# Kernel tuning notes

Hardware: AMD Instinct MI355X
Metric: run time of the kernel (lower is better)

The kernel has to match this reference:

```python
import jax, jax.numpy as jnp
import numpy as np

# ---- model constants (match init_kwargs) ----
N_USERS = 100_000
N_ITEMS = 50_000
N_ENTITIES = 200_000          # items are entities [0, N_ITEMS)
N_REL = 20                    # relations after the +1 shift; rel_weight has N_REL-1 rows
EMB = 64
HOPS = 2
MARGIN_CCL = 0.8
NUM_NEG = 64
ANGLE_W = 0.1
ANGLE_DROP = 0.5              # eval-mode Dropout(ones)*rate == constant rate scaling
N_EDGES = 1_000_000
NNZ = 1_000_000
N_TRIPLETS = 200_000
BATCH = 4096
EPS = 1e-6


def _l2norm(x):
    # torch F.normalize(dim=-1, eps=1e-12)
    return x / jnp.maximum(jnp.linalg.norm(x, axis=-1, keepdims=True), 1e-12)


def setup_inputs() -> dict:
    key = jax.random.key(0)
    ks = jax.random.split(key, 13)
    # xavier_uniform bounds: sqrt(6/(fan_in+fan_out))
    b_all = float(np.sqrt(6.0 / (N_USERS + N_ENTITIES + EMB)))
    b_cf = float(np.sqrt(6.0 / (N_ITEMS + EMB)))
    b_rel = float(np.sqrt(6.0 / (N_REL - 1 + EMB)))
    all_embed = jax.random.uniform(ks[0], (N_USERS + N_ENTITIES, EMB), jnp.float32, -b_all, b_all)
    item_emb_cf = jax.random.uniform(ks[1], (N_ITEMS, EMB), jnp.float32, -b_cf, b_cf)
    rel_weight = jax.random.uniform(ks[2], (N_REL - 1, EMB), jnp.float32, -b_rel, b_rel)
    # D^{-1/2} A row-normalized positive values
    interact_vals = jax.random.uniform(ks[3], (NNZ,), jnp.float32, 0.01, 0.3)
    user = jax.random.randint(ks[4], (BATCH,), 0, N_USERS)
    pos_item = jax.random.randint(ks[5], (BATCH,), 0, N_ITEMS)
    neg_item = jax.random.randint(ks[6], (BATCH, NUM_NEG), 0, N_ITEMS)
    edge_index = jax.random.randint(ks[7], (2, N_EDGES), 0, N_ENTITIES)
    edge_type = jax.random.randint(ks[8], (N_EDGES,), 1, N_REL)  # relations already +1 shifted
    interact_rows = jax.random.randint(ks[9], (NNZ,), 0, N_USERS)
    interact_cols = jax.random.randint(ks[10], (NNZ,), 0, N_ITEMS)  # URM cols live in item range
    triplet_h = jax.random.randint(ks[11], (N_TRIPLETS,), 0, N_ENTITIES)
    triplet_t = jax.random.randint(ks[12], (N_TRIPLETS,), 0, N_ITEMS)
    return dict(all_embed=all_embed, item_emb_cf=item_emb_cf, rel_weight=rel_weight,
                interact_vals=interact_vals, user=user, pos_item=pos_item, neg_item=neg_item,
                edge_index=edge_index, edge_type=edge_type, interact_rows=interact_rows,
                interact_cols=interact_cols, triplet_h=triplet_h, triplet_t=triplet_t)


def _gcn(user_emb, entity_emb, item_cf, rel_weight, edge_index, edge_type, rows, cols, vals):
    """Multi-hop HAKG GraphConv: relation-gated KG scatter-mean + sparse user/CF aggregation."""
    head, tail = edge_index[0], edge_index[1]
    ent_res, usr_res, cf_res = entity_emb, user_emb, item_cf
    cnt = jax.ops.segment_sum(jnp.ones(head.shape, entity_emb.dtype), head, N_ENTITIES)
    denom = jnp.maximum(cnt, 1.0)[:, None]            # scatter_mean denominator
    rel_e = rel_weight[edge_type - 1]                 # [E, D]
    for _ in range(HOPS):
        # KG aggregate: entity_agg[h] = mean_{(h,r,t)} entity[t] * rel[r]
        neigh = entity_emb[tail] * rel_e              # [E, D]
        entity_agg = jax.ops.segment_sum(neigh, head, N_ENTITIES) / denom
        # user aggregate: sparse interact_mat @ entity_emb
        user_agg = jax.ops.segment_sum(vals[:, None] * entity_emb[cols], rows, N_USERS)
        # CF branch (LightGCN-style): R @ item_cf then R^T @ (...)
        u_cf = jax.ops.segment_sum(vals[:, None] * item_cf[cols], rows, N_USERS)
        item_agg_cf = jax.ops.segment_sum(vals[:, None] * u_cf[rows], cols, N_ITEMS)
        entity_emb = _l2norm(entity_agg)
        user_emb = _l2norm(user_agg)
        item_cf = _l2norm(item_agg_cf)
        ent_res = ent_res + entity_emb
        usr_res = usr_res + user_emb
        cf_res = cf_res + item_cf
    return ent_res, usr_res, cf_res


def _half_aperture(u):
    K = 0.1
    sqnu = jnp.clip(jnp.sum(u * u, -1), 0.0, 1.0 - EPS)
    return jnp.arcsin(jnp.clip(K * (1.0 - sqnu) / jnp.sqrt(sqnu), -1.0 + EPS, 1.0 - EPS))


def _angle_at_u(u, v):
    nu = jnp.linalg.norm(u, axis=-1)
    nv = jnp.linalg.norm(v, axis=-1)
    dp = jnp.sum(u * v, -1)
    ed = jnp.linalg.norm(u - v, axis=-1)
    num = dp * (1.0 + nu ** 2) - nu ** 2 * (1.0 + nv ** 2)
    den = nu * ed * jnp.sqrt(jnp.clip(1.0 + nv ** 2 * nu ** 2 - 2.0 * dp, EPS, None)) + EPS
    return jnp.arccos(jnp.clip(num / den, -1.0 + EPS, 1.0 - EPS))


def _contrastive_loss(u_e, pos_e, neg_e, pos_cf, neg_cf):
    B = u_e.shape[0]
    u, p, n = _l2norm(u_e), _l2norm(pos_e), _l2norm(neg_e)
    pcf, ncf = _l2norm(pos_cf), _l2norm(neg_cf)
    ui_pos = jax.nn.relu(2.0 - (jnp.sum(u * p, -1) + jnp.sum(u * pcf, -1)))
    ub = jnp.repeat(u, NUM_NEG, axis=0)               # [B*K, D]
    def neg_loss(nn_):
        s = jax.nn.relu(jnp.sum(ub * nn_, -1) - MARGIN_CCL).reshape(B, NUM_NEG)
        return jnp.sum(s, -1) / (jnp.sum(s > 0, -1).astype(s.dtype) + 1e-5)
    return jnp.mean(ui_pos + neg_loss(n) + neg_loss(ncf))


def reference(all_embed, item_emb_cf, rel_weight, interact_vals, user, pos_item, neg_item,
              edge_index, edge_type, interact_rows, interact_cols, triplet_h, triplet_t):
    user_emb = all_embed[:N_USERS]
    entity_emb = all_embed[N_USERS:]
    ent_g, usr_g, cf_g = _gcn(user_emb, entity_emb, item_emb_cf, rel_weight,
                              edge_index, edge_type, interact_rows, interact_cols, interact_vals)
    flat_neg = neg_item.reshape(-1)
    u_e = usr_g[user]
    loss1 = _contrastive_loss(u_e, ent_g[pos_item], ent_g[flat_neg], cf_g[pos_item], cf_g[flat_neg])
    # angle (hierarchy) loss, vectorized over all cross-type triplets
    hs = entity_emb[triplet_h] * ANGLE_DROP
    ts = entity_emb[triplet_t] * ANGLE_DROP
    angle_half = jax.nn.relu(_angle_at_u(hs, ts) - _half_aperture(hs))
    loss2 = ANGLE_W * jnp.sum(angle_half) / N_TRIPLETS
    return loss1 + loss2
```

## Files before the change

### kernel.cpp

```cpp
#include <hip/hip_runtime.h>
#include <math.h>

#define N_USERS    100000
#define N_ITEMS    50000
#define N_ENTITIES 200000
#define N_REL      20
#define EMB        64
#define HOPS       2
#define MARGIN_CCL 0.8f
#define NUM_NEG    64
#define ANGLE_W    0.1f
#define ANGLE_DROP 0.5f
#define N_EDGES    1000000
#define NNZ        1000000
#define N_TRIPLETS 200000
#define BATCH      4096
#define EPSF       1e-6f

#define TILE1 4096
#define NBUCK 196
#define BCAP  9216
#define ACAP  8192
#define HBLK  ((N_EDGES + TILE1 - 1) / TILE1)
#define KGB   (N_ENTITIES / 32)
#define USERB (N_USERS / 16)
#define ITEMB ((N_ITEMS + 31) / 32)
#define ANGB  (N_TRIPLETS / 32)
#define LOSSB (BATCH / 4)
#define CONVE (N_ENTITIES * 16 / 256)
#define CONVI (N_ITEMS * 16 / 256)

typedef _Float16 half4_t __attribute__((ext_vector_type(4)));
typedef _Float16 half8_t __attribute__((ext_vector_type(8)));
typedef float float8_t __attribute__((ext_vector_type(8)));

__device__ inline float4 h2f(half4_t h) {
    return make_float4((float)h.x, (float)h.y, (float)h.z, (float)h.w);
}
__device__ inline half4_t f2h(float4 f) {
    half4_t h; h.x = (_Float16)f.x; h.y = (_Float16)f.y;
    h.z = (_Float16)f.z; h.w = (_Float16)f.w; return h;
}
__device__ inline float8_t h8_to_f8(half8_t h) { return __builtin_convertvector(h, float8_t); }
__device__ inline half8_t f8_to_h8(float8_t f) { return __builtin_convertvector(f, half8_t); }
__device__ inline half8_t h8_zero() {
    half8_t z;
    #pragma unroll
    for (int i = 0; i < 8; ++i) z[i] = (_Float16)0.0f;
    return z;
}
__device__ inline float sum_sq8(float8_t f) {
    float s = 0.f;
    #pragma unroll
    for (int i = 0; i < 8; ++i) s += f[i] * f[i];
    return s;
}
__device__ inline float dot8(float8_t a, float8_t b) {
    float s = 0.f;
    #pragma unroll
    for (int i = 0; i < 8; ++i) s += a[i] * b[i];
    return s;
}
__device__ inline float8_t f8_from2(float4 lo, float4 hi) {
    float8_t f;
    f[0] = lo.x; f[1] = lo.y; f[2] = lo.z; f[3] = lo.w;
    f[4] = hi.x; f[5] = hi.y; f[6] = hi.z; f[7] = hi.w;
    return f;
}
__device__ inline float grp_red8(float v) {
    v += __shfl_xor(v, 1, 64); v += __shfl_xor(v, 2, 64); v += __shfl_xor(v, 4, 64);
    return v;
}
__device__ inline float dot4(float4 a, float4 b) {
    return a.x * b.x + a.y * b.y + a.z * b.z + a.w * b.w;
}
__device__ inline float grp_red16(float v) {
    v += __shfl_xor(v, 1, 64); v += __shfl_xor(v, 2, 64);
    v += __shfl_xor(v, 4, 64); v += __shfl_xor(v, 8, 64);
    return v;
}
__device__ inline float cross_grp_scalar(float v) {
    v += __shfl_xor(v, 16, 64); v += __shfl_xor(v, 32, 64);
    return v;
}

__global__ void __launch_bounds__(256) prep_kernel(
        const float4* __restrict__ ent0, const float4* __restrict__ cf0,
        half4_t* __restrict__ ent_a, half4_t* __restrict__ comb_a,
        int* __restrict__ bcur_e, int* __restrict__ bcur_u, int* __restrict__ bcur_i) {
    int bx = blockIdx.x, t = threadIdx.x;
    if (bx < CONVE) { int i = bx * 256 + t; ent_a[i] = f2h(ent0[i]); return; }
    bx -= CONVE;
    if (bx < CONVI) {
        int i = bx * 256 + t;
        int row = i >> 4, o4 = i & 15;
        comb_a[row * 32 + o4] = f2h(ent0[i]);
        return;
    }
    bx -= CONVI;
    if (bx < CONVI) {
        int i = bx * 256 + t;
        int row = i >> 4, o4 = i & 15;
        comb_a[row * 32 + 16 + o4] = f2h(cf0[i]);
        return;
    }
    if (t < NBUCK) {
        bcur_e[t] = t * ACAP;
        bcur_u[t] = t * ACAP;
        bcur_i[t] = t * ACAP;
    }
}

__global__ void __launch_bounds__(256) phase1_all(
        const int* __restrict__ head, const int* __restrict__ tail,
        const int* __restrict__ etype, const int* __restrict__ rows,
        const int* __restrict__ cols, const float* __restrict__ vals,
        int* __restrict__ bcur_e, int* __restrict__ bcur_u, int* __restrict__ bcur_i,
        int* __restrict__ keys_e, int* __restrict__ kg_pay,
        int* __restrict__ keys_u, int2* __restrict__ u_pay,
        int* __restrict__ keys_i, int2* __restrict__ i_pay) {
    __shared__ int lhist[256], lstart[256], lcur[256], gbase[256];
    __shared__ int key_st[TILE1];
    __shared__ int2 pay_st[TILE1];
    int seg = blockIdx.x / HBLK;
    int tb  = blockIdx.x % HBLK;
    int t = threadIdx.x;
    int tstart = tb * TILE1;
    int valid = min(TILE1, N_EDGES - tstart);
    const int* karr = (seg == 0) ? head : (seg == 1) ? rows : cols;
    int shift = (seg == 0) ? 10 : (seg == 1) ? 9 : 8;
    int* bcur = (seg == 0) ? bcur_e : (seg == 1) ? bcur_u : bcur_i;
    lhist[t] = 0;
    __syncthreads();
    for (int i = t; i < valid; i += 256) atomicAdd(&lhist[karr[tstart + i] >> shift], 1);
    __syncthreads();
    int v = lhist[t];
    lstart[t] = v;
    __syncthreads();
    for (int d = 1; d < 256; d <<= 1) {
        int x = (t >= d) ? lstart[t - d] : 0;
        __syncthreads();
        lstart[t] += x;
        __syncthreads();
    }
    int excl = lstart[t] - v;
    lstart[t] = excl;
    lcur[t] = excl;
    gbase[t] = atomicAdd(&bcur[t], v);
    __syncthreads();
    if (seg == 0) {
        int* ps = (int*)pay_st;
        for (int i = t; i < valid; i += 256) {
            int h = head[tstart + i];
            int p = tail[tstart + i] | ((etype[tstart + i] - 1) << 18);
            int sp = atomicAdd(&lcur[h >> 10], 1);
            key_st[sp] = h;
            ps[sp] = p;
        }
        __syncthreads();
        for (int j = t; j < valid; j += 256) {
            int k = key_st[j];
            int b = k >> 10;
            int pos = gbase[b] + (j - lstart[b]);
            keys_e[pos] = k;
            kg_pay[pos] = ps[j];
        }
    } else {
        const int* oth = (seg == 1) ? cols : rows;
        int* keys = (seg == 1) ? keys_u : keys_i;
        int2* pay = (seg == 1) ? u_pay : i_pay;
        for (int i = t; i < valid; i += 256) {
            int k = karr[tstart + i];
            int2 p = make_int2(oth[tstart + i], __float_as_int(vals[tstart + i]));
            int sp = atomicAdd(&lcur[k >> shift], 1);
            key_st[sp] = k;
            pay_st[sp] = p;
        }
        __syncthreads();
        for (int j = t; j < valid; j += 256) {
            int k = key_st[j];
            int b = k >> shift;
            int pos = gbase[b] + (j - lstart[b]);
            keys[pos] = k;
            pay[pos] = pay_st[j];
        }
    }
}

__global__ void __launch_bounds__(256) phase2_all(
        const int* __restrict__ bcur_e, const int* __restrict__ keys_e,
        int* __restrict__ kg_pay, int* __restrict__ off_e,
        const int* __restrict__ bcur_u, const int* __restrict__ keys_u,
        int2* __restrict__ u_pay, int* __restrict__ off_u,
        const int* __restrict__ bcur_i, const int* __restrict__ keys_i,
        int2* __restrict__ i_pay, int* __restrict__ off_i) {
    __shared__ int hist[1024];
    __shared__ int s[256];
    __shared__ int2 lout2[BCAP];
    int seg = blockIdx.x / NBUCK;
    int b   = blockIdx.x % NBUCK;
    int t = threadIdx.x;
    int bins  = (seg == 0) ? 1024 : (seg == 1) ? 512 : 256;
    int shift = (seg == 0) ? 10 : (seg == 1) ? 9 : 8;
    int n_rows = (seg == 0) ? N_ENTITIES : (seg == 1) ? N_USERS : N_ITEMS;
    const int* bcur = (seg == 0) ? bcur_e : (seg == 1) ? bcur_u : bcur_i;
    const int* keys = (seg == 0) ? keys_e : (seg == 1) ? keys_u : keys_i;
    int* off = (seg == 0) ? off_e : (seg == 1) ? off_u : off_i;
    int rs = b << shift;
    int re = min(rs + bins, n_rows);
    int nr = re - rs;
    int base = b * ACAP;
    int len = bcur[b] - base;
    for (int r = t; r < bins; r += 256) hist[r] = 0;
    __syncthreads();
    for (int j = t; j < len; j += 256) atomicAdd(&hist[keys[base + j] - rs], 1);
    __syncthreads();
    int own = bins >> 8;
    int c[4]; int tot = 0;
    #pragma unroll 4
    for (int i = 0; i < own; ++i) { c[i] = hist[t * own + i]; tot += c[i]; }
    s[t] = tot;
    __syncthreads();
    for (int d = 1; d < 256; d <<= 1) {
        int x = (t >= d) ? s[t - d] : 0;
        __syncthreads();
        s[t] += x;
        __syncthreads();
    }
    int run = s[t] - tot;
    #pragma unroll 4
    for (int i = 0; i < own; ++i) { hist[t * own + i] = run; run += c[i]; }
    __syncthreads();
    for (int r = t; r < nr; r += 256) off[rs + b + r] = base + hist[r];
    if (t == 0) off[rs + b + nr] = base + len;
    __syncthreads();
    if (seg == 0) {
        int* lo = (int*)lout2;
        for (int j = t; j < len; j += 256) {
            int k = keys[base + j];
            int slot = atomicAdd(&hist[k - rs], 1);
            lo[slot] = kg_pay[base + j];
        }
        __syncthreads();
        for (int j = t; j < len; j += 256) kg_pay[base + j] = lo[j];
    } else {
        int2* pay = (seg == 1) ? u_pay : i_pay;
        for (int j = t; j < len; j += 256) {
            int k = keys[base + j];
            int slot = atomicAdd(&hist[k - rs], 1);
            lout2[slot] = pay[base + j];
        }
        __syncthreads();
        for (int j = t; j < len; j += 256) pay[base + j] = lout2[j];
    }
}

__device__ inline void kg_body(int bid, int t, const int* __restrict__ off,
                               const int* __restrict__ pack, half8_t* srel,
                               const float* __restrict__ relw,
                               const half8_t* __restrict__ src, half8_t* __restrict__ dst,
                               half8_t* __restrict__ comb_nxt, half8_t* __restrict__ res,
                               const float4* __restrict__ res_init, int first, int last) {
    if (t < (N_REL - 1) * 8) {
        int rel = t >> 3, o = t & 7;
        const float4* r4 = (const float4*)relw;
        srel[rel * 9 + o] = f8_to_h8(f8_from2(r4[rel * 16 + o * 2], r4[rel * 16 + o * 2 + 1]));
    }
    __syncthreads();
    int row = bid * 32 + (t >> 3);
    int o = t & 7;
    int idx = row + (row >> 10);
    int s = off[idx], e = off[idx + 1];
    half8_t acc = h8_zero();
    int k = s;
    for (; k + 2 <= e; k += 2) {
        int p0 = pack[k], p1 = pack[k + 1];
        half8_t a0 = src[(p0 & 0x3FFFF) * 8 + o];
        half8_t b0 = srel[(p0 >> 18) * 9 + o];
        half8_t a1 = src[(p1 & 0x3FFFF) * 8 + o];
        half8_t b1 = srel[(p1 >> 18) * 9 + o];
        acc += a0 * b0;
        acc += a1 * b1;
    }
    if (k < e) {
        int p0 = pack[k];
        acc += src[(p0 & 0x3FFFF) * 8 + o] * srel[(p0 >> 18) * 9 + o];
    }
    float8_t f = h8_to_f8(acc);
    f *= 1.0f / fmaxf((float)(e - s), 1.0f);
    float ss = grp_red8(sum_sq8(f));
    f *= 1.0f / fmaxf(sqrtf(ss), 1e-12f);
    half8_t oh = f8_to_h8(f);
    dst[row * 8 + o] = oh;
    if (row < N_ITEMS) {
        if (!last) comb_nxt[row * 16 + o] = oh;
        float8_t rr;
        if (first) rr = f8_from2(res_init[row * 16 + o * 2], res_init[row * 16 + o * 2 + 1]);
        else       rr = h8_to_f8(res[row * 8 + o]);
        rr += f;
        if (last) {
            float s2 = grp_red8(sum_sq8(rr));
            rr *= 1.0f / fmaxf(sqrtf(s2), 1e-12f);
        }
        res[row * 8 + o] = f8_to_h8(rr);
    }
}

__device__ inline void user_body(int bid, int t, const int* __restrict__ off,
                                 const int2* __restrict__ u_pack,
                                 const half8_t* __restrict__ comb,
                                 half8_t* __restrict__ usr_res,
                                 const float4* __restrict__ res_init,
                                 half8_t* __restrict__ ucf, int first, int last) {
    int row = bid * 16 + (t >> 4);
    int o = t & 15;
    int idx = row + (row >> 9);
    int s = off[idx], e = off[idx + 1];
    half8_t acc = h8_zero();
    int k = s;
    for (; k + 2 <= e; k += 2) {
        int2 p0 = u_pack[k], p1 = u_pack[k + 1];
        _Float16 v0 = (_Float16)__int_as_float(p0.y);
        _Float16 v1 = (_Float16)__int_as_float(p1.y);
        acc += comb[p0.x * 16 + o] * v0;
        acc += comb[p1.x * 16 + o] * v1;
    }
    if (k < e) {
        int2 p0 = u_pack[k];
        acc += comb[p0.x * 16 + o] * (_Float16)__int_as_float(p0.y);
    }
    float8_t f = h8_to_f8(acc);
    float ss = grp_red8(sum_sq8(f));
    if (o < 8) {
        float rn = 1.0f / fmaxf(sqrtf(ss), 1e-12f);
        float8_t rr;
        if (first) rr = f8_from2(res_init[row * 16 + o * 2], res_init[row * 16 + o * 2 + 1]);
        else       rr = h8_to_f8(usr_res[row * 8 + o]);
        rr += f * rn;
        if (last) {
            float s2 = grp_red8(sum_sq8(rr));
            rr *= 1.0f / fmaxf(sqrtf(s2), 1e-12f);
        }
        usr_res[row * 8 + o] = f8_to_h8(rr);
    } else {
        ucf[row * 8 + (o - 8)] = acc;
    }
}

__device__ inline void item_body(int bid, int t, const int* __restrict__ off,
                                 const int2* __restrict__ i_pack,
                                 const half8_t* __restrict__ ucf,
                                 half8_t* __restrict__ comb_nxt, half8_t* __restrict__ res,
                                 const float4* __restrict__ res_init, int first, int last) {
    int row = bid * 32 + (t >> 3);
    int o = t & 7;
    if (row >= N_ITEMS) return;
    int idx = row + (row >> 8);
    int s = off[idx], e = off[idx + 1];
    half8_t acc = h8_zero();
    int k = s;
    for (; k + 2 <= e; k += 2) {
        int2 p0 = i_pack[k], p1 = i_pack[k + 1];
        _Float16 v0 = (_Float16)__int_as_float(p0.y);
        _Float16 v1 = (_Float16)__int_as_float(p1.y);
        acc += ucf[p0.x * 8 + o] * v0;
        acc += ucf[p1.x * 8 + o] * v1;
    }
    if (k < e) {
        int2 p0 = i_pack[k];
        acc += ucf[p0.x * 8 + o] * (_Float16)__int_as_float(p0.y);
    }
    float8_t f = h8_to_f8(acc);
    float ss = grp_red8(sum_sq8(f));
    f *= 1.0f / fmaxf(sqrtf(ss), 1e-12f);
    if (!last) comb_nxt[row * 16 + 8 + o] = f8_to_h8(f);
    float8_t rr;
    if (first) rr = f8_from2(res_init[row * 16 + o * 2], res_init[row * 16 + o * 2 + 1]);
    else       rr = h8_to_f8(res[row * 8 + o]);
    rr += f;
    if (last) {
        float s2 = grp_red8(sum_sq8(rr));
        rr *= 1.0f / fmaxf(sqrtf(s2), 1e-12f);
    }
    res[row * 8 + o] = f8_to_h8(rr);
}

__device__ inline void angle_body(int ablk, int t, const half8_t* __restrict__ ent_h,
                                  const int* __restrict__ th, const int* __restrict__ tt,
                                  float* sb, float* __restrict__ l2blk) {
    int o = t & 7;
    int grp = t >> 3;
    int trip = ablk * 32 + grp;
    int h = th[trip], t2 = tt[trip];
    float8_t hv = h8_to_f8(ent_h[h * 8 + o]);
    float8_t tv = h8_to_f8(ent_h[t2 * 8 + o]);
    hv *= ANGLE_DROP;
    tv *= ANGLE_DROP;
    float8_t dv = hv - tv;
    float s_hh = grp_red8(sum_sq8(hv));
    float s_tt = grp_red8(sum_sq8(tv));
    float s_ht = grp_red8(dot8(hv, tv));
    float s_dd = grp_red8(sum_sq8(dv));
    if (o == 0) {
        float nu = sqrtf(s_hh);
        float ed = sqrtf(s_dd);
        float sqnu = fminf(fmaxf(s_hh, 0.0f), 1.0f - EPSF);
        float ha_arg = fminf(fmaxf(0.1f * (1.0f - sqnu) / sqrtf(sqnu), -1.0f + EPSF), 1.0f - EPSF);
        float half_ap = asinf(ha_arg);
        float num = s_ht * (1.0f + s_hh) - s_hh * (1.0f + s_tt);
        float den = nu * ed * sqrtf(fmaxf(1.0f + s_tt * s_hh - 2.0f * s_ht, EPSF)) + EPSF;
        float ang = acosf(fminf(fmaxf(num / den, -1.0f + EPSF), 1.0f - EPSF));
        sb[grp] = fmaxf(ang - half_ap, 0.0f);
    }
    __syncthreads();
    if (t == 0) {
        float tot = 0.f;
        #pragma unroll
        for (int i = 0; i < 32; ++i) tot += sb[i];
        l2blk[ablk] = tot;
    }
}

__device__ inline void loss_ent_body(int b, int t, const int* __restrict__ user,
                                     const int* __restrict__ pos, const int* __restrict__ neg,
                                     const half4_t* __restrict__ usr4,
                                     const half4_t* __restrict__ ent4,
                                     float* __restrict__ dpe, float* __restrict__ l1pe) {
    int lane = t & 63;
    int g = lane >> 4, q = lane & 15;
    int uid = user[b], pid = pos[b];
    float4 u = h2f(usr4[uid * 16 + q]);
    float4 p = h2f(ent4[pid * 16 + q]);
    float dpe_v = grp_red16(dot4(u, p));
    float sum_n = 0.f, cnt_n = 0.f;
    const int* nb = neg + b * NUM_NEG;
    for (int j = 0; j < NUM_NEG; j += 8) {
        int n0 = nb[j + g], n1 = nb[j + 4 + g];
        float dn0 = grp_red16(dot4(u, h2f(ent4[n0 * 16 + q])));
        float dn1 = grp_red16(dot4(u, h2f(ent4[n1 * 16 + q])));
        float s0 = fmaxf(dn0 - MARGIN_CCL, 0.f); sum_n += s0; if (s0 > 0.f) cnt_n += 1.f;
        float s1 = fmaxf(dn1 - MARGIN_CCL, 0.f); sum_n += s1; if (s1 > 0.f) cnt_n += 1.f;
    }
    sum_n = cross_grp_scalar(sum_n); cnt_n = cross_grp_scalar(cnt_n);
    if (lane == 0) {
        dpe[b] = dpe_v;
        l1pe[b] = sum_n / (cnt_n + 1e-5f);
    }
}

__global__ void __launch_bounds__(256) loss_cf_kernel(
        const int* __restrict__ user, const int* __restrict__ pos,
        const int* __restrict__ neg, const half4_t* __restrict__ usr4,
        const half4_t* __restrict__ cf4, const float* __restrict__ dpe,
        const float* __restrict__ l1pe, float* __restrict__ l1p) {
    int b = blockIdx.x * 4 + (threadIdx.x >> 6);
    int lane = threadIdx.x & 63;
    int g = lane >> 4, q = lane & 15;
    int uid = user[b], pid = pos[b];
    float4 u = h2f(usr4[uid * 16 + q]);
    float4 pc = h2f(cf4[pid * 16 + q]);
    float dpc = grp_red16(dot4(u, pc));
    float sum_c = 0.f, cnt_c = 0.f;
    const int* nb = neg + b * NUM_NEG;
    for (int j = 0; j < NUM_NEG; j += 8) {
        int n0 = nb[j + g], n1 = nb[j + 4 + g];
        float dc0 = grp_red16(dot4(u, h2f(cf4[n0 * 16 + q])));
        float dc1 = grp_red16(dot4(u, h2f(cf4[n1 * 16 + q])));
        float t0 = fmaxf(dc0 - MARGIN_CCL, 0.f); sum_c += t0; if (t0 > 0.f) cnt_c += 1.f;
        float t1 = fmaxf(dc1 - MARGIN_CCL, 0.f); sum_c += t1; if (t1 > 0.f) cnt_c += 1.f;
    }
    sum_c = cross_grp_scalar(sum_c); cnt_c = cross_grp_scalar(cnt_c);
    if (lane == 0) {
        float ui_pos = fmaxf(2.0f - dpe[b] - dpc, 0.0f);
        l1p[b] = ui_pos + l1pe[b] + sum_c / (cnt_c + 1e-5f);
    }
}

__global__ void __launch_bounds__(256) fused_h0(
        const int* __restrict__ off_e, const int* __restrict__ kg_pack,
        const float* __restrict__ relw, const half8_t* __restrict__ ent_a,
        half8_t* __restrict__ ent_b, half8_t* __restrict__ comb_b,
        half8_t* __restrict__ ent_res, const float4* __restrict__ ent0f,
        const int* __restrict__ off_u, const int2* __restrict__ u_pack,
        const half8_t* __restrict__ comb_a, half8_t* __restrict__ usr_res,
        const float4* __restrict__ usr0f, half8_t* __restrict__ ucf,
        const int* __restrict__ th, const int* __restrict__ tt,
        float* __restrict__ l2blk) {
    __shared__ half8_t srel[(N_REL - 1) * 9];
    __shared__ float sb[32];
    int bx = blockIdx.x, t = threadIdx.x;
    if (bx < KGB) {
        kg_body(bx, t, off_e, kg_pack, srel, relw, ent_a, ent_b, comb_b, ent_res, ent0f, 1, 0);
    } else if (bx < KGB + USERB) {
        user_body(bx - KGB, t, off_u, u_pack, comb_a, usr_res, usr0f, ucf, 1, 0);
    } else {
        angle_body(bx - KGB - USERB, t, ent_a, th, tt, sb, l2blk);
    }
}

__global__ void __launch_bounds__(256) fused_ik(
        const int* __restrict__ off_e, const int* __restrict__ kg_pack,
        const float* __restrict__ relw, const half8_t* __restrict__ ent_b,
        half8_t* __restrict__ ent_a, half8_t* __restrict__ ent_res,
        const float4* __restrict__ ent0f,
        const int* __restrict__ off_i, const int2* __restrict__ i_pack,
        const half8_t* __restrict__ ucf, half8_t* __restrict__ comb_b,
        half8_t* __restrict__ cf_res, const float4* __restrict__ cf0f) {
    __shared__ half8_t srel[(N_REL - 1) * 9];
    int bx = blockIdx.x, t = threadIdx.x;
    if (bx < KGB) {
        kg_body(bx, t, off_e, kg_pack, srel, relw, ent_b, ent_a, comb_b, ent_res, ent0f, 0, 1);
    } else {
        item_body(bx - KGB, t, off_i, i_pack, ucf, comb_b, cf_res, cf0f, 1, 0);
    }
}

__global__ void __launch_bounds__(256) user_h1(
        const int* __restrict__ off_u, const int2* __restrict__ u_pack,
        const half8_t* __restrict__ comb_b, half8_t* __restrict__ usr_res,
        const float4* __restrict__ usr0f, half8_t* __restrict__ ucf) {
    user_body(blockIdx.x, threadIdx.x, off_u, u_pack, comb_b, usr_res, usr0f, ucf, 0, 1);
}

__global__ void __launch_bounds__(256) fused_item_loss(
        const int* __restrict__ off_i, const int2* __restrict__ i_pack,
        const half8_t* __restrict__ ucf, half8_t* __restrict__ comb_unused,
        half8_t* __restrict__ cf_res, const float4* __restrict__ cf0f,
        const int* __restrict__ user, const int* __restrict__ pos,
        const int* __restrict__ neg, const half4_t* __restrict__ usr4,
        const half4_t* __restrict__ ent4, float* __restrict__ dpe,
        float* __restrict__ l1pe) {
    int bx = blockIdx.x, t = threadIdx.x;
    if (bx < ITEMB) {
        item_body(bx, t, off_i, i_pack, ucf, comb_unused, cf_res, cf0f, 0, 1);
    } else {
        int b = (bx - ITEMB) * 4 + (t >> 6);
        loss_ent_body(b, t, user, pos, neg, usr4, ent4, dpe, l1pe);
    }
}

__global__ void finalize_kernel(const float* __restrict__ l1p, const float* __restrict__ l2b,
                                float* __restrict__ out) {
    __shared__ float sb[1024];
    float a1 = 0.f;
    for (int i = threadIdx.x; i < BATCH; i += 1024) a1 += l1p[i];
    float a2 = 0.f;
    for (int i = threadIdx.x; i < ANGB; i += 1024) a2 += l2b[i];
    sb[threadIdx.x] = a1 / (float)BATCH + ANGLE_W * a2 / (float)N_TRIPLETS;
    __syncthreads();
    for (int s = 512; s > 0; s >>= 1) {
        if (threadIdx.x < s) sb[threadIdx.x] += sb[threadIdx.x + s];
        __syncthreads();
    }
    if (threadIdx.x == 0) out[0] = sb[0];
}

extern "C" void kernel_launch(void* const* d_in, const int* in_sizes, int n_in,
                              void* d_out, int out_size, void* d_ws, size_t ws_size,
                              hipStream_t stream) {
    const float* all_embed = (const float*)d_in[0];
    const float* item_cf0  = (const float*)d_in[1];
    const float* relw      = (const float*)d_in[2];
    const float* vals      = (const float*)d_in[3];
    const int* user        = (const int*)d_in[4];
    const int* pos_item    = (const int*)d_in[5];
    const int* neg_item    = (const int*)d_in[6];
    const int* edge_head   = (const int*)d_in[7];
    const int* edge_tail   = edge_head + N_EDGES;
    const int* etype       = (const int*)d_in[8];
    const int* irows       = (const int*)d_in[9];
    const int* icols       = (const int*)d_in[10];
    const int* th          = (const int*)d_in[11];
    const int* tt          = (const int*)d_in[12];
    float* out             = (float*)d_out;

    char* base = (char*)d_ws;
    size_t woff = 0;
    auto alloc = [&](size_t bytes) -> void* {
        void* p = base + woff;
        woff = (woff + bytes + 255) & ~(size_t)255;
        return p;
    };
    half8_t* ent_a   = (half8_t*)alloc((size_t)N_ENTITIES * EMB * 2);
    half8_t* ent_b   = (half8_t*)alloc((size_t)N_ENTITIES * EMB * 2);
    half8_t* comb_a  = (half8_t*)alloc((size_t)N_ITEMS * EMB * 4);
    half8_t* comb_b  = (half8_t*)alloc((size_t)N_ITEMS * EMB * 4);
    half8_t* ucf     = (half8_t*)alloc((size_t)N_USERS * EMB * 2);
    half8_t* ent_res = (half8_t*)alloc((size_t)N_ITEMS * EMB * 2);
    half8_t* usr_res = (half8_t*)alloc((size_t)N_USERS * EMB * 2);
    half8_t* cf_res  = (half8_t*)alloc((size_t)N_ITEMS * EMB * 2);
    int2* u_pack     = (int2*)alloc((size_t)NBUCK * ACAP * 8);
    int2* i_pack     = (int2*)alloc((size_t)NBUCK * ACAP * 8);
    int* kg_pack     = (int*)alloc((size_t)NBUCK * ACAP * 4);
    int* keys_e      = (int*)alloc((size_t)NBUCK * ACAP * 4);
    int* keys_u      = (int*)alloc((size_t)NBUCK * ACAP * 4);
    int* keys_i      = (int*)alloc((size_t)NBUCK * ACAP * 4);
    float* l1p       = (float*)alloc((size_t)BATCH * 4);
    float* dpe       = (float*)alloc((size_t)BATCH * 4);
    float* l1pe      = (float*)alloc((size_t)BATCH * 4);
    float* l2blk     = (float*)alloc((size_t)ANGB * 4);
    int* off_e       = (int*)alloc((size_t)(N_ENTITIES + NBUCK + 1) * 4);
    int* off_u       = (int*)alloc((size_t)(N_USERS + NBUCK + 1) * 4);
    int* off_i       = (int*)alloc((size_t)(N_ITEMS + NBUCK + 1) * 4);
    int* bcur_e      = (int*)alloc(256 * 4);
    int* bcur_u      = (int*)alloc(256 * 4);
    int* bcur_i      = (int*)alloc(256 * 4);

    const float* ent0 = all_embed + (size_t)N_USERS * EMB;

    prep_kernel<<<CONVE + 2 * CONVI + 1, 256, 0, stream>>>(
        (const float4*)ent0, (const float4*)item_cf0, (half4_t*)ent_a, (half4_t*)comb_a,
        bcur_e, bcur_u, bcur_i);
    phase1_all<<<3 * HBLK, 256, 0, stream>>>(edge_head, edge_tail, etype, irows, icols, vals,
                                             bcur_e, bcur_u, bcur_i,
                                             keys_e, kg_pack, keys_u, u_pack, keys_i, i_pack);
    phase2_all<<<3 * NBUCK, 256, 0, stream>>>(bcur_e, keys_e, kg_pack, off_e,
                                              bcur_u, keys_u, u_pack, off_u,
                                              bcur_i, keys_i, i_pack, off_i);
    fused_h0<<<KGB + USERB + ANGB, 256, 0, stream>>>(
        off_e, kg_pack, relw, ent_a, ent_b, comb_b, ent_res, (const float4*)ent0,
        off_u, u_pack, comb_a, usr_res, (const float4*)all_embed, ucf,
        th, tt, l2blk);
    fused_ik<<<KGB + ITEMB, 256, 0, stream>>>(
        off_e, kg_pack, relw, ent_b, ent_a, ent_res, (const float4*)ent0,
        off_i, i_pack, ucf, comb_b, cf_res, (const float4*)item_cf0);
    user_h1<<<USERB, 256, 0, stream>>>(off_u, u_pack, comb_b, usr_res,
                                       (const float4*)all_embed, ucf);
    fused_item_loss<<<ITEMB + LOSSB, 256, 0, stream>>>(
        off_i, i_pack, ucf, comb_a, cf_res, (const float4*)item_cf0,
        user, pos_item, neg_item, (const half4_t*)usr_res, (const half4_t*)ent_res,
        dpe, l1pe);
    loss_cf_kernel<<<LOSSB, 256, 0, stream>>>(user, pos_item, neg_item,
                                              (const half4_t*)usr_res, (const half4_t*)cf_res,
                                              dpe, l1pe, l1p);
    finalize_kernel<<<1, 1024, 0, stream>>>(l1p, l2blk, out);
}
```

Baseline: 424.0 us.

## Pack sort keys into payloads and move angle loss into phase1 launch

The low bits of the user and item sort keys are packed into the high bits of the payload index. This removes the separate keys_u/keys_i arrays and their global writes and reads in phase1 and phase2, and the scatter in phase1 now finds each element's bucket with a binary search over lstart. The angle-loss blocks move from fused_h0 into the phase1 launch, so they run alongside the bucketing work. The cost is extra masking in the user and item gather loops and a 256-entry binary search per element, and it assumes the column indices fit in 16 or 17 bits.

```diff
diff --git a/kernel.cpp b/kernel.cpp
--- a/kernel.cpp
+++ b/kernel.cpp
@@ -22,6 +22,7 @@
 #define BCAP  9216
 #define ACAP  8192
 #define HBLK  ((N_EDGES + TILE1 - 1) / TILE1)
+#define P1B   (3 * HBLK)
 #define KGB   (N_ENTITIES / 32)
 #define USERB (N_USERS / 16)
 #define ITEMB ((N_ITEMS + 31) / 32)
@@ -109,280 +110,6 @@
         bcur_u[t] = t * ACAP;
         bcur_i[t] = t * ACAP;
     }
-}
-
-__global__ void __launch_bounds__(256) phase1_all(
-        const int* __restrict__ head, const int* __restrict__ tail,
-        const int* __restrict__ etype, const int* __restrict__ rows,
-        const int* __restrict__ cols, const float* __restrict__ vals,
-        int* __restrict__ bcur_e, int* __restrict__ bcur_u, int* __restrict__ bcur_i,
-        int* __restrict__ keys_e, int* __restrict__ kg_pay,
-        int* __restrict__ keys_u, int2* __restrict__ u_pay,
-        int* __restrict__ keys_i, int2* __restrict__ i_pay) {
-    __shared__ int lhist[256], lstart[256], lcur[256], gbase[256];
-    __shared__ int key_st[TILE1];
-    __shared__ int2 pay_st[TILE1];
-    int seg = blockIdx.x / HBLK;
-    int tb  = blockIdx.x % HBLK;
-    int t = threadIdx.x;
-    int tstart = tb * TILE1;
-    int valid = min(TILE1, N_EDGES - tstart);
-    const int* karr = (seg == 0) ? head : (seg == 1) ? rows : cols;
-    int shift = (seg == 0) ? 10 : (seg == 1) ? 9 : 8;
-    int* bcur = (seg == 0) ? bcur_e : (seg == 1) ? bcur_u : bcur_i;
-    lhist[t] = 0;
-    __syncthreads();
-    for (int i = t; i < valid; i += 256) atomicAdd(&lhist[karr[tstart + i] >> shift], 1);
-    __syncthreads();
-    int v = lhist[t];
-    lstart[t] = v;
-    __syncthreads();
-    for (int d = 1; d < 256; d <<= 1) {
-        int x = (t >= d) ? lstart[t - d] : 0;
-        __syncthreads();
-        lstart[t] += x;
-        __syncthreads();
-    }
-    int excl = lstart[t] - v;
-    lstart[t] = excl;
-    lcur[t] = excl;
-    gbase[t] = atomicAdd(&bcur[t], v);
-    __syncthreads();
-    if (seg == 0) {
-        int* ps = (int*)pay_st;
-        for (int i = t; i < valid; i += 256) {
-            int h = head[tstart + i];
-            int p = tail[tstart + i] | ((etype[tstart + i] - 1) << 18);
-            int sp = atomicAdd(&lcur[h >> 10], 1);
-            key_st[sp] = h;
-            ps[sp] = p;
-        }
-        __syncthreads();
-        for (int j = t; j < valid; j += 256) {
-            int k = key_st[j];
-            int b = k >> 10;
-            int pos = gbase[b] + (j - lstart[b]);
-            keys_e[pos] = k;
-            kg_pay[pos] = ps[j];
-        }
-    } else {
-        const int* oth = (seg == 1) ? cols : rows;
-        int* keys = (seg == 1) ? keys_u : keys_i;
-        int2* pay = (seg == 1) ? u_pay : i_pay;
-        for (int i = t; i < valid; i += 256) {
-            int k = karr[tstart + i];
-            int2 p = make_int2(oth[tstart + i], __float_as_int(vals[tstart + i]));
-            int sp = atomicAdd(&lcur[k >> shift], 1);
-            key_st[sp] = k;
-            pay_st[sp] = p;
-        }
-        __syncthreads();
-        for (int j = t; j < valid; j += 256) {
-            int k = key_st[j];
-            int b = k >> shift;
-            int pos = gbase[b] + (j - lstart[b]);
-            keys[pos] = k;
-            pay[pos] = pay_st[j];
-        }
-    }
-}
-
-__global__ void __launch_bounds__(256) phase2_all(
-        const int* __restrict__ bcur_e, const int* __restrict__ keys_e,
-        int* __restrict__ kg_pay, int* __restrict__ off_e,
-        const int* __restrict__ bcur_u, const int* __restrict__ keys_u,
-        int2* __restrict__ u_pay, int* __restrict__ off_u,
-        const int* __restrict__ bcur_i, const int* __restrict__ keys_i,
-        int2* __restrict__ i_pay, int* __restrict__ off_i) {
-    __shared__ int hist[1024];
-    __shared__ int s[256];
-    __shared__ int2 lout2[BCAP];
-    int seg = blockIdx.x / NBUCK;
-    int b   = blockIdx.x % NBUCK;
-    int t = threadIdx.x;
-    int bins  = (seg == 0) ? 1024 : (seg == 1) ? 512 : 256;
-    int shift = (seg == 0) ? 10 : (seg == 1) ? 9 : 8;
-    int n_rows = (seg == 0) ? N_ENTITIES : (seg == 1) ? N_USERS : N_ITEMS;
-    const int* bcur = (seg == 0) ? bcur_e : (seg == 1) ? bcur_u : bcur_i;
-    const int* keys = (seg == 0) ? keys_e : (seg == 1) ? keys_u : keys_i;
-    int* off = (seg == 0) ? off_e : (seg == 1) ? off_u : off_i;
-    int rs = b << shift;
-    int re = min(rs + bins, n_rows);
-    int nr = re - rs;
-    int base = b * ACAP;
-    int len = bcur[b] - base;
-    for (int r = t; r < bins; r += 256) hist[r] = 0;
-    __syncthreads();
-    for (int j = t; j < len; j += 256) atomicAdd(&hist[keys[base + j] - rs], 1);
-    __syncthreads();
-    int own = bins >> 8;
-    int c[4]; int tot = 0;
-    #pragma unroll 4
-    for (int i = 0; i < own; ++i) { c[i] = hist[t * own + i]; tot += c[i]; }
-    s[t] = tot;
-    __syncthreads();
-    for (int d = 1; d < 256; d <<= 1) {
-        int x = (t >= d) ? s[t - d] : 0;
-        __syncthreads();
-        s[t] += x;
-        __syncthreads();
-    }
-    int run = s[t] - tot;
-    #pragma unroll 4
-    for (int i = 0; i < own; ++i) { hist[t * own + i] = run; run += c[i]; }
-    __syncthreads();
-    for (int r = t; r < nr; r += 256) off[rs + b + r] = base + hist[r];
-    if (t == 0) off[rs + b + nr] = base + len;
-    __syncthreads();
-    if (seg == 0) {
-        int* lo = (int*)lout2;
-        for (int j = t; j < len; j += 256) {
-            int k = keys[base + j];
-            int slot = atomicAdd(&hist[k - rs], 1);
-            lo[slot] = kg_pay[base + j];
-        }
-        __syncthreads();
-        for (int j = t; j < len; j += 256) kg_pay[base + j] = lo[j];
-    } else {
-        int2* pay = (seg == 1) ? u_pay : i_pay;
-        for (int j = t; j < len; j += 256) {
-            int k = keys[base + j];
-            int slot = atomicAdd(&hist[k - rs], 1);
-            lout2[slot] = pay[base + j];
-        }
-        __syncthreads();
-        for (int j = t; j < len; j += 256) pay[base + j] = lout2[j];
-    }
-}
-
-__device__ inline void kg_body(int bid, int t, const int* __restrict__ off,
-                               const int* __restrict__ pack, half8_t* srel,
-                               const float* __restrict__ relw,
-                               const half8_t* __restrict__ src, half8_t* __restrict__ dst,
-                               half8_t* __restrict__ comb_nxt, half8_t* __restrict__ res,
-                               const float4* __restrict__ res_init, int first, int last) {
-    if (t < (N_REL - 1) * 8) {
-        int rel = t >> 3, o = t & 7;
-        const float4* r4 = (const float4*)relw;
-        srel[rel * 9 + o] = f8_to_h8(f8_from2(r4[rel * 16 + o * 2], r4[rel * 16 + o * 2 + 1]));
-    }
-    __syncthreads();
-    int row = bid * 32 + (t >> 3);
-    int o = t & 7;
-    int idx = row + (row >> 10);
-    int s = off[idx], e = off[idx + 1];
-    half8_t acc = h8_zero();
-    int k = s;
-    for (; k + 2 <= e; k += 2) {
-        int p0 = pack[k], p1 = pack[k + 1];
-        half8_t a0 = src[(p0 & 0x3FFFF) * 8 + o];
-        half8_t b0 = srel[(p0 >> 18) * 9 + o];
-        half8_t a1 = src[(p1 & 0x3FFFF) * 8 + o];
-        half8_t b1 = srel[(p1 >> 18) * 9 + o];
-        acc += a0 * b0;
-        acc += a1 * b1;
-    }
-    if (k < e) {
-        int p0 = pack[k];
-        acc += src[(p0 & 0x3FFFF) * 8 + o] * srel[(p0 >> 18) * 9 + o];
-    }
-    float8_t f = h8_to_f8(acc);
-    f *= 1.0f / fmaxf((float)(e - s), 1.0f);
-    float ss = grp_red8(sum_sq8(f));
-    f *= 1.0f / fmaxf(sqrtf(ss), 1e-12f);
-    half8_t oh = f8_to_h8(f);
-    dst[row * 8 + o] = oh;
-    if (row < N_ITEMS) {
-        if (!last) comb_nxt[row * 16 + o] = oh;
-        float8_t rr;
-        if (first) rr = f8_from2(res_init[row * 16 + o * 2], res_init[row * 16 + o * 2 + 1]);
-        else       rr = h8_to_f8(res[row * 8 + o]);
-        rr += f;
-        if (last) {
-            float s2 = grp_red8(sum_sq8(rr));
-            rr *= 1.0f / fmaxf(sqrtf(s2), 1e-12f);
-        }
-        res[row * 8 + o] = f8_to_h8(rr);
-    }
-}
-
-__device__ inline void user_body(int bid, int t, const int* __restrict__ off,
-                                 const int2* __restrict__ u_pack,
-                                 const half8_t* __restrict__ comb,
-                                 half8_t* __restrict__ usr_res,
-                                 const float4* __restrict__ res_init,
-                                 half8_t* __restrict__ ucf, int first, int last) {
-    int row = bid * 16 + (t >> 4);
-    int o = t & 15;
-    int idx = row + (row >> 9);
-    int s = off[idx], e = off[idx + 1];
-    half8_t acc = h8_zero();
-    int k = s;
-    for (; k + 2 <= e; k += 2) {
-        int2 p0 = u_pack[k], p1 = u_pack[k + 1];
-        _Float16 v0 = (_Float16)__int_as_float(p0.y);
-        _Float16 v1 = (_Float16)__int_as_float(p1.y);
-        acc += comb[p0.x * 16 + o] * v0;
-        acc += comb[p1.x * 16 + o] * v1;
-    }
-    if (k < e) {
-        int2 p0 = u_pack[k];
-        acc += comb[p0.x * 16 + o] * (_Float16)__int_as_float(p0.y);
-    }
-    float8_t f = h8_to_f8(acc);
-    float ss = grp_red8(sum_sq8(f));
-    if (o < 8) {
-        float rn = 1.0f / fmaxf(sqrtf(ss), 1e-12f);
-        float8_t rr;
-        if (first) rr = f8_from2(res_init[row * 16 + o * 2], res_init[row * 16 + o * 2 + 1]);
-        else       rr = h8_to_f8(usr_res[row * 8 + o]);
-        rr += f * rn;
-        if (last) {
-            float s2 = grp_red8(sum_sq8(rr));
-            rr *= 1.0f / fmaxf(sqrtf(s2), 1e-12f);
-        }
-        usr_res[row * 8 + o] = f8_to_h8(rr);
-    } else {
-        ucf[row * 8 + (o - 8)] = acc;
-    }
-}
-
-__device__ inline void item_body(int bid, int t, const int* __restrict__ off,
-                                 const int2* __restrict__ i_pack,
-                                 const half8_t* __restrict__ ucf,
-                                 half8_t* __restrict__ comb_nxt, half8_t* __restrict__ res,
-                                 const float4* __restrict__ res_init, int first, int last) {
-    int row = bid * 32 + (t >> 3);
-    int o = t & 7;
-    if (row >= N_ITEMS) return;
-    int idx = row + (row >> 8);
-    int s = off[idx], e = off[idx + 1];
-    half8_t acc = h8_zero();
-    int k = s;
-    for (; k + 2 <= e; k += 2) {
-        int2 p0 = i_pack[k], p1 = i_pack[k + 1];
-        _Float16 v0 = (_Float16)__int_as_float(p0.y);
-        _Float16 v1 = (_Float16)__int_as_float(p1.y);
-        acc += ucf[p0.x * 8 + o] * v0;
-        acc += ucf[p1.x * 8 + o] * v1;
-    }
-    if (k < e) {
-        int2 p0 = i_pack[k];
-        acc += ucf[p0.x * 8 + o] * (_Float16)__int_as_float(p0.y);
-    }
-    float8_t f = h8_to_f8(acc);
-    float ss = grp_red8(sum_sq8(f));
-    f *= 1.0f / fmaxf(sqrtf(ss), 1e-12f);
-    if (!last) comb_nxt[row * 16 + 8 + o] = f8_to_h8(f);
-    float8_t rr;
-    if (first) rr = f8_from2(res_init[row * 16 + o * 2], res_init[row * 16 + o * 2 + 1]);
-    else       rr = h8_to_f8(res[row * 8 + o]);
-    rr += f;
-    if (last) {
-        float s2 = grp_red8(sum_sq8(rr));
-        rr *= 1.0f / fmaxf(sqrtf(s2), 1e-12f);
-    }
-    res[row * 8 + o] = f8_to_h8(rr);
 }
 
 __device__ inline void angle_body(int ablk, int t, const half8_t* __restrict__ ent_h,
@@ -421,6 +148,298 @@
     }
 }
 
+__global__ void __launch_bounds__(256) phase1_angle(
+        const int* __restrict__ head, const int* __restrict__ tail,
+        const int* __restrict__ etype, const int* __restrict__ rows,
+        const int* __restrict__ cols, const float* __restrict__ vals,
+        int* __restrict__ bcur_e, int* __restrict__ bcur_u, int* __restrict__ bcur_i,
+        int* __restrict__ keys_e, int* __restrict__ kg_pay,
+        int2* __restrict__ u_pay, int2* __restrict__ i_pay,
+        const half8_t* __restrict__ ent_a, const int* __restrict__ th,
+        const int* __restrict__ tt, float* __restrict__ l2blk) {
+    __shared__ int2 pay_st[TILE1];
+    __shared__ int lhist[256], lstart[256], lcur[256], gbase[256];
+    __shared__ float sb[32];
+    int bx = blockIdx.x, t = threadIdx.x;
+    if (bx >= P1B) {
+        angle_body(bx - P1B, t, ent_a, th, tt, sb, l2blk);
+        return;
+    }
+    int seg = bx / HBLK;
+    int tb  = bx % HBLK;
+    int tstart = tb * TILE1;
+    int valid = min(TILE1, N_EDGES - tstart);
+    const int* karr = (seg == 0) ? head : (seg == 1) ? rows : cols;
+    int shift = (seg == 0) ? 10 : (seg == 1) ? 9 : 8;
+    int* bcur = (seg == 0) ? bcur_e : (seg == 1) ? bcur_u : bcur_i;
+    lhist[t] = 0;
+    __syncthreads();
+    for (int i = t; i < valid; i += 256) atomicAdd(&lhist[karr[tstart + i] >> shift], 1);
+    __syncthreads();
+    int v = lhist[t];
+    lstart[t] = v;
+    __syncthreads();
+    for (int d = 1; d < 256; d <<= 1) {
+        int x = (t >= d) ? lstart[t - d] : 0;
+        __syncthreads();
+        lstart[t] += x;
+        __syncthreads();
+    }
+    int excl = lstart[t] - v;
+    lstart[t] = excl;
+    lcur[t] = excl;
+    gbase[t] = atomicAdd(&bcur[t], v);
+    __syncthreads();
+    if (seg == 0) {
+        int* key_st = (int*)pay_st;
+        int* ps = key_st + TILE1;
+        for (int i = t; i < valid; i += 256) {
+            int h = head[tstart + i];
+            int p = tail[tstart + i] | ((etype[tstart + i] - 1) << 18);
+            int sp = atomicAdd(&lcur[h >> 10], 1);
+            key_st[sp] = h;
+            ps[sp] = p;
+        }
+        __syncthreads();
+        for (int j = t; j < valid; j += 256) {
+            int k = key_st[j];
+            int b = k >> 10;
+            int pos = gbase[b] + (j - lstart[b]);
+            keys_e[pos] = k;
+            kg_pay[pos] = ps[j];
+        }
+    } else {
+        int2* pay = (seg == 1) ? u_pay : i_pay;
+        for (int i = t; i < valid; i += 256) {
+            int k = karr[tstart + i];
+            int px;
+            if (seg == 1) px = cols[tstart + i] | ((k & 511) << 16);
+            else          px = rows[tstart + i] | ((k & 255) << 17);
+            int2 p = make_int2(px, __float_as_int(vals[tstart + i]));
+            int sp = atomicAdd(&lcur[k >> shift], 1);
+            pay_st[sp] = p;
+        }
+        __syncthreads();
+        for (int j = t; j < valid; j += 256) {
+            int2 p = pay_st[j];
+            int key = (seg == 1) ? ((p.x >> 16) & 511) : ((p.x >> 17) & 255);
+            int b = (gbase[0], 0);
+            (void)b;
+            int lo = 0, hi = 255;
+            while (lo < hi) {
+                int mid = (lo + hi + 1) >> 1;
+                if (lstart[mid] <= j) lo = mid; else hi = mid - 1;
+            }
+            int bb = lo;
+            int pos = gbase[bb] + (j - lstart[bb]);
+            pay[pos] = p;
+        }
+    }
+}
+
+__global__ void __launch_bounds__(256) phase2_all(
+        const int* __restrict__ bcur_e, const int* __restrict__ keys_e,
+        int* __restrict__ kg_pay, int* __restrict__ off_e,
+        const int* __restrict__ bcur_u, int2* __restrict__ u_pay, int* __restrict__ off_u,
+        const int* __restrict__ bcur_i, int2* __restrict__ i_pay, int* __restrict__ off_i) {
+    __shared__ int hist[1024];
+    __shared__ int s[256];
+    __shared__ int2 lout2[BCAP];
+    int seg = blockIdx.x / NBUCK;
+    int b   = blockIdx.x % NBUCK;
+    int t = threadIdx.x;
+    int bins  = (seg == 0) ? 1024 : (seg == 1) ? 512 : 256;
+    int shift = (seg == 0) ? 10 : (seg == 1) ? 9 : 8;
+    int n_rows = (seg == 0) ? N_ENTITIES : (seg == 1) ? N_USERS : N_ITEMS;
+    const int* bcur = (seg == 0) ? bcur_e : (seg == 1) ? bcur_u : bcur_i;
+    int* off = (seg == 0) ? off_e : (seg == 1) ? off_u : off_i;
+    int rs = b << shift;
+    int re = min(rs + bins, n_rows);
+    int nr = re - rs;
+    int base = b * ACAP;
+    int len = bcur[b] - base;
+    for (int r = t; r < bins; r += 256) hist[r] = 0;
+    __syncthreads();
+    if (seg == 0) {
+        for (int j = t; j < len; j += 256) atomicAdd(&hist[keys_e[base + j] - rs], 1);
+    } else if (seg == 1) {
+        for (int j = t; j < len; j += 256) atomicAdd(&hist[(u_pay[base + j].x >> 16) & 511], 1);
+    } else {
+        for (int j = t; j < len; j += 256) atomicAdd(&hist[(i_pay[base + j].x >> 17) & 255], 1);
+    }
+    __syncthreads();
+    int own = bins >> 8;
+    int c[4]; int tot = 0;
+    #pragma unroll 4
+    for (int i = 0; i < own; ++i) { c[i] = hist[t * own + i]; tot += c[i]; }
+    s[t] = tot;
+    __syncthreads();
+    for (int d = 1; d < 256; d <<= 1) {
+        int x = (t >= d) ? s[t - d] : 0;
+        __syncthreads();
+        s[t] += x;
+        __syncthreads();
+    }
+    int run = s[t] - tot;
+    #pragma unroll 4
+    for (int i = 0; i < own; ++i) { hist[t * own + i] = run; run += c[i]; }
+    __syncthreads();
+    for (int r = t; r < nr; r += 256) off[rs + b + r] = base + hist[r];
+    if (t == 0) off[rs + b + nr] = base + len;
+    __syncthreads();
+    if (seg == 0) {
+        int* lo = (int*)lout2;
+        for (int j = t; j < len; j += 256) {
+            int k = keys_e[base + j];
+            int slot = atomicAdd(&hist[k - rs], 1);
+            lo[slot] = kg_pay[base + j];
+        }
+        __syncthreads();
+        for (int j = t; j < len; j += 256) kg_pay[base + j] = lo[j];
+    } else {
+        int2* pay = (seg == 1) ? u_pay : i_pay;
+        int sh = (seg == 1) ? 16 : 17;
+        int msk = (seg == 1) ? 511 : 255;
+        for (int j = t; j < len; j += 256) {
+            int2 p = pay[base + j];
+            int slot = atomicAdd(&hist[(p.x >> sh) & msk], 1);
+            lout2[slot] = p;
+        }
+        __syncthreads();
+        for (int j = t; j < len; j += 256) pay[base + j] = lout2[j];
+    }
+}
+
+__device__ inline void kg_body(int bid, int t, const int* __restrict__ off,
+                               const int* __restrict__ pack, half8_t* srel,
+                               const float* __restrict__ relw,
+                               const half8_t* __restrict__ src, half8_t* __restrict__ dst,
+                               half8_t* __restrict__ comb_nxt, half8_t* __restrict__ res,
+                               const float4* __restrict__ res_init, int first, int last) {
+    if (t < (N_REL - 1) * 8) {
+        int rel = t >> 3, o = t & 7;
+        const float4* r4 = (const float4*)relw;
+        srel[rel * 9 + o] = f8_to_h8(f8_from2(r4[rel * 16 + o * 2], r4[rel * 16 + o * 2 + 1]));
+    }
+    __syncthreads();
+    int row = bid * 32 + (t >> 3);
+    int o = t & 7;
+    int idx = row + (row >> 10);
+    int s = off[idx], e = off[idx + 1];
+    half8_t acc = h8_zero();
+    int k = s;
+    for (; k + 2 <= e; k += 2) {
+        int p0 = pack[k], p1 = pack[k + 1];
+        half8_t a0 = src[(p0 & 0x3FFFF) * 8 + o];
+        half8_t b0 = srel[(p0 >> 18) * 9 + o];
+        half8_t a1 = src[(p1 & 0x3FFFF) * 8 + o];
+        half8_t b1 = srel[(p1 >> 18) * 9 + o];
+        acc += a0 * b0;
+        acc += a1 * b1;
+    }
+    if (k < e) {
+        int p0 = pack[k];
+        acc += src[(p0 & 0x3FFFF) * 8 + o] * srel[(p0 >> 18) * 9 + o];
+    }
+    float8_t f = h8_to_f8(acc);
+    f *= 1.0f / fmaxf((float)(e - s), 1.0f);
+    float ss = grp_red8(sum_sq8(f));
+    f *= 1.0f / fmaxf(sqrtf(ss), 1e-12f);
+    half8_t oh = f8_to_h8(f);
+    dst[row * 8 + o] = oh;
+    if (row < N_ITEMS) {
+        if (!last) comb_nxt[row * 16 + o] = oh;
+        float8_t rr;
+        if (first) rr = f8_from2(res_init[row * 16 + o * 2], res_init[row * 16 + o * 2 + 1]);
+        else       rr = h8_to_f8(res[row * 8 + o]);
+        rr += f;
+        if (last) {
+            float s2 = grp_red8(sum_sq8(rr));
+            rr *= 1.0f / fmaxf(sqrtf(s2), 1e-12f);
+        }
+        res[row * 8 + o] = f8_to_h8(rr);
+    }
+}
+
+__device__ inline void user_body(int bid, int t, const int* __restrict__ off,
+                                 const int2* __restrict__ u_pack,
+                                 const half8_t* __restrict__ comb,
+                                 half8_t* __restrict__ usr_res,
+                                 const float4* __restrict__ res_init,
+                                 half8_t* __restrict__ ucf, int first, int last) {
+    int row = bid * 16 + (t >> 4);
+    int o = t & 15;
+    int idx = row + (row >> 9);
+    int s = off[idx], e = off[idx + 1];
+    half8_t acc = h8_zero();
+    int k = s;
+    for (; k + 2 <= e; k += 2) {
+        int2 p0 = u_pack[k], p1 = u_pack[k + 1];
+        _Float16 v0 = (_Float16)__int_as_float(p0.y);
+        _Float16 v1 = (_Float16)__int_as_float(p1.y);
+        acc += comb[(p0.x & 0xFFFF) * 16 + o] * v0;
+        acc += comb[(p1.x & 0xFFFF) * 16 + o] * v1;
+    }
+    if (k < e) {
+        int2 p0 = u_pack[k];
+        acc += comb[(p0.x & 0xFFFF) * 16 + o] * (_Float16)__int_as_float(p0.y);
+    }
+    float8_t f = h8_to_f8(acc);
+    float ss = grp_red8(sum_sq8(f));
+    if (o < 8) {
+        float rn = 1.0f / fmaxf(sqrtf(ss), 1e-12f);
+        float8_t rr;
+        if (first) rr = f8_from2(res_init[row * 16 + o * 2], res_init[row * 16 + o * 2 + 1]);
+        else       rr = h8_to_f8(usr_res[row * 8 + o]);
+        rr += f * rn;
+        if (last) {
+            float s2 = grp_red8(sum_sq8(rr));
+            rr *= 1.0f / fmaxf(sqrtf(s2), 1e-12f);
+        }
+        usr_res[row * 8 + o] = f8_to_h8(rr);
+    } else {
+        ucf[row * 8 + (o - 8)] = acc;
+    }
+}
+
+__device__ inline void item_body(int bid, int t, const int* __restrict__ off,
+                                 const int2* __restrict__ i_pack,
+                                 const half8_t* __restrict__ ucf,
+                                 half8_t* __restrict__ comb_nxt, half8_t* __restrict__ res,
+                                 const float4* __restrict__ res_init, int first, int last) {
+    int row = bid * 32 + (t >> 3);
+    int o = t & 7;
+    if (row >= N_ITEMS) return;
+    int idx = row + (row >> 8);
+    int s = off[idx], e = off[idx + 1];
+    half8_t acc = h8_zero();
+    int k = s;
+    for (; k + 2 <= e; k += 2) {
+        int2 p0 = i_pack[k], p1 = i_pack[k + 1];
+        _Float16 v0 = (_Float16)__int_as_float(p0.y);
+        _Float16 v1 = (_Float16)__int_as_float(p1.y);
+        acc += ucf[(p0.x & 0x1FFFF) * 8 + o] * v0;
+        acc += ucf[(p1.x & 0x1FFFF) * 8 + o] * v1;
+    }
+    if (k < e) {
+        int2 p0 = i_pack[k];
+        acc += ucf[(p0.x & 0x1FFFF) * 8 + o] * (_Float16)__int_as_float(p0.y);
+    }
+    float8_t f = h8_to_f8(acc);
+    float ss = grp_red8(sum_sq8(f));
+    f *= 1.0f / fmaxf(sqrtf(ss), 1e-12f);
+    if (!last) comb_nxt[row * 16 + 8 + o] = f8_to_h8(f);
+    float8_t rr;
+    if (first) rr = f8_from2(res_init[row * 16 + o * 2], res_init[row * 16 + o * 2 + 1]);
+    else       rr = h8_to_f8(res[row * 8 + o]);
+    rr += f;
+    if (last) {
+        float s2 = grp_red8(sum_sq8(rr));
+        rr *= 1.0f / fmaxf(sqrtf(s2), 1e-12f);
+    }
+    res[row * 8 + o] = f8_to_h8(rr);
+}
+
 __device__ inline void loss_ent_body(int b, int t, const int* __restrict__ user,
                                      const int* __restrict__ pos, const int* __restrict__ neg,
                                      const half4_t* __restrict__ usr4,
@@ -483,18 +502,13 @@
         half8_t* __restrict__ ent_res, const float4* __restrict__ ent0f,
         const int* __restrict__ off_u, const int2* __restrict__ u_pack,
         const half8_t* __restrict__ comb_a, half8_t* __restrict__ usr_res,
-        const float4* __restrict__ usr0f, half8_t* __restrict__ ucf,
-        const int* __restrict__ th, const int* __restrict__ tt,
-        float* __restrict__ l2blk) {
+        const float4* __restrict__ usr0f, half8_t* __restrict__ ucf) {
     __shared__ half8_t srel[(N_REL - 1) * 9];
-    __shared__ float sb[32];
     int bx = blockIdx.x, t = threadIdx.x;
     if (bx < KGB) {
         kg_body(bx, t, off_e, kg_pack, srel, relw, ent_a, ent_b, comb_b, ent_res, ent0f, 1, 0);
-    } else if (bx < KGB + USERB) {
+    } else {
         user_body(bx - KGB, t, off_u, u_pack, comb_a, usr_res, usr0f, ucf, 1, 0);
-    } else {
-        angle_body(bx - KGB - USERB, t, ent_a, th, tt, sb, l2blk);
     }
 }
 
@@ -593,8 +607,6 @@
     int2* i_pack     = (int2*)alloc((size_t)NBUCK * ACAP * 8);
     int* kg_pack     = (int*)alloc((size_t)NBUCK * ACAP * 4);
     int* keys_e      = (int*)alloc((size_t)NBUCK * ACAP * 4);
-    int* keys_u      = (int*)alloc((size_t)NBUCK * ACAP * 4);
-    int* keys_i      = (int*)alloc((size_t)NBUCK * ACAP * 4);
     float* l1p       = (float*)alloc((size_t)BATCH * 4);
     float* dpe       = (float*)alloc((size_t)BATCH * 4);
     float* l1pe      = (float*)alloc((size_t)BATCH * 4);
@@ -611,16 +623,16 @@
     prep_kernel<<<CONVE + 2 * CONVI + 1, 256, 0, stream>>>(
         (const float4*)ent0, (const float4*)item_cf0, (half4_t*)ent_a, (half4_t*)comb_a,
         bcur_e, bcur_u, bcur_i);
-    phase1_all<<<3 * HBLK, 256, 0, stream>>>(edge_head, edge_tail, etype, irows, icols, vals,
-                                             bcur_e, bcur_u, bcur_i,
-                                             keys_e, kg_pack, keys_u, u_pack, keys_i, i_pack);
+    phase1_angle<<<P1B + ANGB, 256, 0, stream>>>(
+        edge_head, edge_tail, etype, irows, icols, vals,
+        bcur_e, bcur_u, bcur_i, keys_e, kg_pack, u_pack, i_pack,
+        ent_a, th, tt, l2blk);
     phase2_all<<<3 * NBUCK, 256, 0, stream>>>(bcur_e, keys_e, kg_pack, off_e,
-                                              bcur_u, keys_u, u_pack, off_u,
-                                              bcur_i, keys_i, i_pack, off_i);
-    fused_h0<<<KGB + USERB + ANGB, 256, 0, stream>>>(
+                                              bcur_u, u_pack, off_u,
+                                              bcur_i, i_pack, off_i);
+    fused_h0<<<KGB + USERB, 256, 0, stream>>>(
         off_e, kg_pack, relw, ent_a, ent_b, comb_b, ent_res, (const float4*)ent0,
-        off_u, u_pack, comb_a, usr_res, (const float4*)all_embed, ucf,
-        th, tt, l2blk);
+        off_u, u_pack, comb_a, usr_res, (const float4*)all_embed, ucf);
     fused_ik<<<KGB + ITEMB, 256, 0, stream>>>(
         off_e, kg_pack, relw, ent_b, ent_a, ent_res, (const float4*)ent0,
         off_i, i_pack, ucf, comb_b, cf_res, (const float4*)item_cf0);
```

Measured after the change: 413.8 us. -2.4%, faster.
